# Kernel tuning notes

Measured on AMD Instinct MI355X. Metric: run time of the kernel, lower is better.

Reference implementation:

```python
import jax, jax.numpy as jnp
import numpy as np

M, K = 16384, 1024
E, N = 8, 5632  # N = 2 * intermediate (gate+up packed); intermediate = 2816
TOPK = 2


def setup_inputs() -> dict:
    key = jax.random.key(0)
    ks = jax.random.split(key, 5)
    return {
        "hidden_states": jax.random.normal(ks[0], (M, K), jnp.float32) * 0.05,
        "w1": jax.random.normal(ks[1], (E, N, K), jnp.float32) * 0.02,
        "w2": jax.random.normal(ks[2], (E, K, N // 2), jnp.float32) * 0.02,
        "topk_weights": jax.random.uniform(ks[3], (M, TOPK), jnp.float32),
        "topk_ids": jax.random.randint(ks[4], (M, TOPK), 0, E, jnp.int32),
    }


def reference(hidden_states, w1, w2, topk_weights, topk_ids):
    # hidden_states: [M, K]; w1: [E, N, K]; w2: [E, K, N//2]
    # topk_weights / topk_ids: [M, TOPK]
    m, k = hidden_states.shape
    e_num, n, _ = w1.shape
    topk = topk_ids.shape[1]
    half = n // 2
    out = jnp.zeros((m, topk, k), dtype=hidden_states.dtype)
    # Loop over the small fixed set of experts; each iteration is a dense GEMM
    # masked by the routing assignment (faithful to the grouped-GEMM math).
    for e in range(e_num):
        h1 = jnp.einsum('mk,nk->mn', hidden_states, w1[e])          # [M, N]
        gate, up = h1[:, :half], h1[:, half:]
        h2 = jax.nn.silu(gate) * up                                  # silu_and_mul
        o = jnp.einsum('mh,kh->mk', h2, w2[e])                       # [M, K]
        mask = (topk_ids == e).astype(o.dtype)                       # [M, TOPK]
        out = out + mask[:, :, None] * o[:, None, :]
    # multiply routed weights and sum over top-k slots
    return jnp.einsum('mtk,mt->mk', out, topk_weights)
```

## Files before the change

kernel.cpp:

```cpp
#include <hip/hip_runtime.h>
#include <hip/hip_bf16.h>

#define M_TOK 16384
#define K_DIM 1024
#define E_NUM 8
#define N_DIM 5632
#define HALF_N 2816
#define TOPK 2
#define NPAIR (M_TOK * TOPK)
#define BM 128
#define BK 64
#define BH1 128
#define BN 128
#define NDESC (NPAIR / BM + E_NUM)
#define NHB1 (HALF_N / BH1)
#define NNB2 (K_DIM / BN)

typedef short s16x4 __attribute__((ext_vector_type(4)));
typedef short s16x8 __attribute__((ext_vector_type(8)));
typedef float f32x4 __attribute__((ext_vector_type(4)));

__device__ __forceinline__ short f2bf(float f) {
  union { __hip_bfloat16 h; short s; } c;
  c.h = __float2bfloat16(f);
  return c.s;
}

__device__ __forceinline__ float bf2f(unsigned short s) {
  union { float f; unsigned u; } c;
  c.u = ((unsigned)s) << 16;
  return c.f;
}

__device__ __forceinline__ void gload_lds16(const void* g, void* l) {
  __builtin_amdgcn_global_load_lds(
      (const __attribute__((address_space(1))) unsigned int*)g,
      (__attribute__((address_space(3))) unsigned int*)l, 16, 0, 0);
}

__device__ __forceinline__ int xcd_work(int bid, int nwg) {
  const int xcd = bid & 7, loc = bid >> 3;
  const int q = nwg >> 3, r = nwg & 7;
  return (xcd < r ? xcd * (q + 1) : r * (q + 1) + (xcd - r) * q) + loc;
}

__global__ void cvt_f32_bf16_k(const float4* __restrict__ src,
                               s16x4* __restrict__ dst, int n4) {
  int i = blockIdx.x * blockDim.x + threadIdx.x;
  int stride = gridDim.x * blockDim.x;
  for (; i < n4; i += stride) {
    float4 f = src[i];
    s16x4 o = { f2bf(f.x), f2bf(f.y), f2bf(f.z), f2bf(f.w) };
    dst[i] = o;
  }
}

__global__ void moe_count(const int* __restrict__ ids, int* __restrict__ cnt) {
  const int p = blockIdx.x * 256 + threadIdx.x;
  const int e = ids[p];
  const int lane = threadIdx.x & 63;
  __shared__ int h[E_NUM];
  if (threadIdx.x < E_NUM) h[threadIdx.x] = 0;
  __syncthreads();
#pragma unroll
  for (int ex = 0; ex < E_NUM; ++ex) {
    unsigned long long m = __ballot(e == ex);
    if (lane == 0 && m) atomicAdd(&h[ex], __popcll(m));
  }
  __syncthreads();
  if (threadIdx.x < E_NUM) atomicAdd(&cnt[threadIdx.x], h[threadIdx.x]);
}

__global__ void moe_build(const int* __restrict__ cnt, int* __restrict__ offs,
                          int4* __restrict__ desc) {
  if (blockIdx.x == 0 && threadIdx.x == 0) {
    int o = 0, d = 0;
    for (int e = 0; e < E_NUM; ++e) {
      offs[e] = o;
      int end = o + cnt[e];
      for (int s = o; s < end; s += BM) desc[d++] = make_int4(e, s, end, 0);
      o = end;
    }
    offs[E_NUM] = o;
    while (d < NDESC) desc[d++] = make_int4(-1, 0, 0, 0);
  }
}

__global__ void moe_scatter(const int* __restrict__ ids, const float* __restrict__ tw,
                            const int* __restrict__ offs, int* __restrict__ fill,
                            int* __restrict__ tok, float* __restrict__ wgt,
                            int* __restrict__ inv) {
  const int p = blockIdx.x * 256 + threadIdx.x;
  const int e = ids[p];
  const int lane = threadIdx.x & 63;
  const int w = threadIdx.x >> 6;
  __shared__ int wcnt[4][E_NUM];
  __shared__ int wpre[4][E_NUM];
  __shared__ int base[E_NUM];
  const unsigned long long lt = (1ull << lane) - 1ull;
  int myrank = 0;
#pragma unroll
  for (int ex = 0; ex < E_NUM; ++ex) {
    unsigned long long m = __ballot(e == ex);
    if (e == ex) myrank = (int)__popcll(m & lt);
    if (lane == 0) wcnt[w][ex] = (int)__popcll(m);
  }
  __syncthreads();
  if (threadIdx.x < E_NUM) {
    const int ex = threadIdx.x;
    int s = 0;
#pragma unroll
    for (int ww = 0; ww < 4; ++ww) { wpre[ww][ex] = s; s += wcnt[ww][ex]; }
    base[ex] = atomicAdd(&fill[ex], s);
  }
  __syncthreads();
  const int pos = offs[e] + base[e] + wpre[w][e] + myrank;
  tok[pos] = p >> 1;
  wgt[pos] = tw[p];
  inv[p] = pos;
}

__global__ void moe_gather(const float* __restrict__ hs, const int* __restrict__ tok,
                           unsigned short* __restrict__ hsb) {
  const int pos = blockIdx.x;
  const int m = tok[pos];
  const int t = threadIdx.x;
  const float4* s = (const float4*)(hs + (size_t)m * K_DIM) + t * 2;
  const float4 a = s[0], b = s[1];
  s16x8 o = { f2bf(a.x), f2bf(a.y), f2bf(a.z), f2bf(a.w),
              f2bf(b.x), f2bf(b.y), f2bf(b.z), f2bf(b.w) };
  *(s16x8*)(hsb + (size_t)pos * K_DIM + t * 8) = o;
}

__launch_bounds__(512)
__global__ void moe_gemm1(const unsigned short* __restrict__ hsb,
                          const unsigned short* __restrict__ w1b,
                          const int4* __restrict__ desc,
                          unsigned short* __restrict__ h2) {
  const int work = xcd_work(blockIdx.x, NHB1 * NDESC);
  const int di = work / NHB1;
  const int hb = work - di * NHB1;
  const int4 d = desc[di];
  const int e = d.x;
  if (e < 0) return;
  const int pos0 = d.y, eend = d.z;
  const int h0 = hb * BH1;

  __shared__ __align__(16) unsigned short As[BM * BK];
  __shared__ __align__(16) unsigned short Gs[BH1 * BK];
  __shared__ __align__(16) unsigned short Us[BH1 * BK];

  const int tid = threadIdx.x;
  const int lane = tid & 63;
  const int wid = tid >> 6;
  const int wr = wid >> 1;
  const int wc = wid & 1;

  const unsigned short* Ab = hsb + (size_t)pos0 * K_DIM;
  const unsigned short* Gb = w1b + ((size_t)e * N_DIM + h0) * K_DIM;
  const unsigned short* Ub = Gb + (size_t)HALF_N * K_DIM;

  f32x4 accg[2][4], accu[2][4];
  const f32x4 z = {0.f, 0.f, 0.f, 0.f};
#pragma unroll
  for (int i = 0; i < 2; ++i)
#pragma unroll
    for (int j = 0; j < 4; ++j) { accg[i][j] = z; accu[i][j] = z; }

  const int lrow = lane >> 3;
  const int scol = ((lane & 7) ^ lrow) << 3;
  const int fr = lane & 15;
  const int fq = lane >> 4;
  const int sw = fr & 7;

  for (int kt = 0; kt < K_DIM / BK; ++kt) {
    const int k0 = kt * BK;
#pragma unroll
    for (int c = 0; c < 2; ++c) {
      const int seg = c * 8 + wid;
      const int row = seg * 8 + lrow;
      gload_lds16(Ab + (size_t)row * K_DIM + k0 + scol, &As[seg * 512]);
      gload_lds16(Gb + (size_t)row * K_DIM + k0 + scol, &Gs[seg * 512]);
      gload_lds16(Ub + (size_t)row * K_DIM + k0 + scol, &Us[seg * 512]);
    }
    __syncthreads();
#pragma unroll
    for (int s = 0; s < 2; ++s) {
      const int coff = (((s * 4 + fq) ^ sw) << 3);
      s16x8 af[2];
#pragma unroll
      for (int i = 0; i < 2; ++i)
        af[i] = *(const s16x8*)&As[(32 * wr + 16 * i + fr) * BK + coff];
#pragma unroll
      for (int j = 0; j < 4; ++j) {
        const int hr = (64 * wc + 16 * j + fr) * BK + coff;
        s16x8 gf = *(const s16x8*)&Gs[hr];
        s16x8 uf = *(const s16x8*)&Us[hr];
#pragma unroll
        for (int i = 0; i < 2; ++i) {
          accg[i][j] = __builtin_amdgcn_mfma_f32_16x16x32_bf16(af[i], gf, accg[i][j], 0, 0, 0);
          accu[i][j] = __builtin_amdgcn_mfma_f32_16x16x32_bf16(af[i], uf, accu[i][j], 0, 0, 0);
        }
      }
    }
    __syncthreads();
  }

  const int vlim = eend - pos0;
#pragma unroll
  for (int i = 0; i < 2; ++i) {
#pragma unroll
    for (int rr = 0; rr < 4; ++rr) {
      const int row = 32 * wr + 16 * i + fq * 4 + rr;
      if (row < vlim) {
        unsigned short* dst = h2 + (size_t)(pos0 + row) * HALF_N + h0 + 64 * wc;
#pragma unroll
        for (int j = 0; j < 4; ++j) {
          const float g = accg[i][j][rr];
          const float u = accu[i][j][rr];
          const float sg = g / (1.0f + __expf(-g));
          dst[16 * j + fr] = (unsigned short)f2bf(sg * u);
        }
      }
    }
  }
}

__launch_bounds__(256)
__global__ void moe_gemm2(const unsigned short* __restrict__ h2,
                          const unsigned short* __restrict__ w2b,
                          const int4* __restrict__ desc,
                          const float* __restrict__ wgt,
                          unsigned short* __restrict__ opair) {
  const int work = xcd_work(blockIdx.x, NNB2 * NDESC);
  const int di = work >> 3;
  const int nb = work & 7;
  const int4 d = desc[di];
  const int e = d.x;
  if (e < 0) return;
  const int pos0 = d.y, eend = d.z;
  const int n0 = nb * BN;

  __shared__ __align__(16) unsigned short As[BM * BK];
  __shared__ __align__(16) unsigned short Bs[BN * BK];

  const int tid = threadIdx.x;
  const int lane = tid & 63;
  const int wid = tid >> 6;
  const int wr = wid >> 1, wc = wid & 1;

  const unsigned short* Ab = h2 + (size_t)pos0 * HALF_N;
  const unsigned short* Bb = w2b + ((size_t)e * K_DIM + n0) * HALF_N;

  f32x4 acc[4][4];
  const f32x4 z = {0.f, 0.f, 0.f, 0.f};
#pragma unroll
  for (int i = 0; i < 4; ++i)
#pragma unroll
    for (int j = 0; j < 4; ++j) acc[i][j] = z;

  const int lrow = lane >> 3;
  const int scol = ((lane & 7) ^ lrow) << 3;
  const int fr = lane & 15;
  const int fq = lane >> 4;
  const int sw = fr & 7;

  for (int ht = 0; ht < HALF_N / BK; ++ht) {
    const int k0 = ht * BK;
#pragma unroll
    for (int c = 0; c < 4; ++c) {
      const int seg = c * 4 + wid;
      const int row = seg * 8 + lrow;
      gload_lds16(Ab + (size_t)row * HALF_N + k0 + scol, &As[seg * 512]);
      gload_lds16(Bb + (size_t)row * HALF_N + k0 + scol, &Bs[seg * 512]);
    }
    __syncthreads();
#pragma unroll
    for (int s = 0; s < 2; ++s) {
      const int coff = (((s * 4 + fq) ^ sw) << 3);
      s16x8 af[4], bf[4];
#pragma unroll
      for (int i = 0; i < 4; ++i)
        af[i] = *(const s16x8*)&As[(64 * wr + 16 * i + fr) * BK + coff];
#pragma unroll
      for (int j = 0; j < 4; ++j)
        bf[j] = *(const s16x8*)&Bs[(64 * wc + 16 * j + fr) * BK + coff];
#pragma unroll
      for (int i = 0; i < 4; ++i)
#pragma unroll
        for (int j = 0; j < 4; ++j)
          acc[i][j] = __builtin_amdgcn_mfma_f32_16x16x32_bf16(af[i], bf[j], acc[i][j], 0, 0, 0);
    }
    __syncthreads();
  }

  const int vlim = eend - pos0;
#pragma unroll
  for (int i = 0; i < 4; ++i) {
#pragma unroll
    for (int rr = 0; rr < 4; ++rr) {
      const int row = 64 * wr + 16 * i + fq * 4 + rr;
      if (row < vlim) {
        const int pos = pos0 + row;
        const float wt = wgt[pos];
        unsigned short* dst = opair + (size_t)pos * K_DIM + n0 + 64 * wc;
#pragma unroll
        for (int j = 0; j < 4; ++j)
          dst[16 * j + fr] = (unsigned short)f2bf(wt * acc[i][j][rr]);
      }
    }
  }
}

__global__ void moe_combine(const unsigned short* __restrict__ opair,
                            const int* __restrict__ inv,
                            float* __restrict__ out) {
  const int m = blockIdx.x;
  const int t = threadIdx.x;
  const int p0 = inv[2 * m], p1 = inv[2 * m + 1];
  const s16x8 a = *(const s16x8*)&opair[(size_t)p0 * K_DIM + t * 8];
  const s16x8 b = *(const s16x8*)&opair[(size_t)p1 * K_DIM + t * 8];
  float4 o0, o1;
  o0.x = bf2f((unsigned short)a[0]) + bf2f((unsigned short)b[0]);
  o0.y = bf2f((unsigned short)a[1]) + bf2f((unsigned short)b[1]);
  o0.z = bf2f((unsigned short)a[2]) + bf2f((unsigned short)b[2]);
  o0.w = bf2f((unsigned short)a[3]) + bf2f((unsigned short)b[3]);
  o1.x = bf2f((unsigned short)a[4]) + bf2f((unsigned short)b[4]);
  o1.y = bf2f((unsigned short)a[5]) + bf2f((unsigned short)b[5]);
  o1.z = bf2f((unsigned short)a[6]) + bf2f((unsigned short)b[6]);
  o1.w = bf2f((unsigned short)a[7]) + bf2f((unsigned short)b[7]);
  float4* dst = (float4*)(out + (size_t)m * K_DIM + t * 8);
  dst[0] = o0;
  dst[1] = o1;
}

__global__ void sentinel_k(float* o) { o[0] = 1.0e9f; }

extern "C" void kernel_launch(void* const* d_in, const int* in_sizes, int n_in,
                              void* d_out, int out_size, void* d_ws, size_t ws_size,
                              hipStream_t stream) {
  const float* hs = (const float*)d_in[0];
  const float* w1 = (const float*)d_in[1];
  const float* w2 = (const float*)d_in[2];
  const float* tw = (const float*)d_in[3];
  const int* ids = (const int*)d_in[4];
  float* out = (float*)d_out;

  char* p = (char*)d_ws;
  auto carve = [&](size_t bytes) {
    char* r = p;
    p += (bytes + 255) & ~(size_t)255;
    return r;
  };
  unsigned short* w1b = (unsigned short*)carve((size_t)E_NUM * N_DIM * K_DIM * 2);
  unsigned short* w2b = (unsigned short*)carve((size_t)E_NUM * K_DIM * HALF_N * 2);
  unsigned short* hsb = (unsigned short*)carve((size_t)(NPAIR + BM) * K_DIM * 2);
  unsigned short* h2  = (unsigned short*)carve((size_t)(NPAIR + BM) * HALF_N * 2);
  int*   tok  = (int*)carve(NPAIR * 4);
  float* wgt  = (float*)carve(NPAIR * 4);
  int*   inv  = (int*)carve(NPAIR * 4);
  int*   meta = (int*)carve(1024);
  int4*  desc = (int4*)carve(NDESC * sizeof(int4));
  size_t need = (size_t)(p - (char*)d_ws);

  unsigned short* opair = hsb;

  if (need > ws_size) {
    hipMemsetAsync(d_out, 0, (size_t)out_size * sizeof(float), stream);
    sentinel_k<<<1, 1, 0, stream>>>(out);
    return;
  }

  int* cnt  = meta;
  int* fill = meta + 64;
  int* offs = meta + 128;

  hipMemsetAsync(meta, 0, 1024, stream);

  cvt_f32_bf16_k<<<2048, 256, 0, stream>>>(
      (const float4*)w1, (s16x4*)w1b, (int)((size_t)E_NUM * N_DIM * K_DIM / 4));
  cvt_f32_bf16_k<<<2048, 256, 0, stream>>>(
      (const float4*)w2, (s16x4*)w2b, (int)((size_t)E_NUM * K_DIM * HALF_N / 4));
  moe_count<<<NPAIR / 256, 256, 0, stream>>>(ids, cnt);
  moe_build<<<1, 64, 0, stream>>>(cnt, offs, desc);
  moe_scatter<<<NPAIR / 256, 256, 0, stream>>>(ids, tw, offs, fill, tok, wgt, inv);
  moe_gather<<<NPAIR, 128, 0, stream>>>(hs, tok, hsb);
  moe_gemm1<<<NHB1 * NDESC, 512, 0, stream>>>(hsb, w1b, desc, h2);
  moe_gemm2<<<NNB2 * NDESC, 256, 0, stream>>>(h2, w2b, desc, wgt, opair);
  moe_combine<<<M_TOK, 128, 0, stream>>>(opair, inv, out);
}
```

Measured before the change: 915.7 us.

## Multi-buffer LDS in both MoE GEMMs to overlap global loads with MFMA

Gemm1 now uses triple-buffered LDS tiles and gemm2 double-buffered tiles. The next tiles are prefetched with direct global-to-LDS loads while MFMA runs on the current tile, and explicit s_waitcnt vmcnt counts plus raw barriers replace the load/sync/compute/sync loop. The goal is to hide global memory latency behind compute. In exchange LDS use grows (about 144KB for gemm1), which can cut occupancy, and correctness depends on the hand-set vmcnt values matching the number of loads issued.

```diff
diff --git a/kernel.cpp b/kernel.cpp
--- a/kernel.cpp
+++ b/kernel.cpp
@@ -146,9 +146,9 @@
   const int pos0 = d.y, eend = d.z;
   const int h0 = hb * BH1;
 
-  __shared__ __align__(16) unsigned short As[BM * BK];
-  __shared__ __align__(16) unsigned short Gs[BH1 * BK];
-  __shared__ __align__(16) unsigned short Us[BH1 * BK];
+  __shared__ __align__(16) unsigned short As[3][BM * BK];
+  __shared__ __align__(16) unsigned short Gs[3][BH1 * BK];
+  __shared__ __align__(16) unsigned short Us[3][BH1 * BK];
 
   const int tid = threadIdx.x;
   const int lane = tid & 63;
@@ -173,29 +173,49 @@
   const int fq = lane >> 4;
   const int sw = fr & 7;
 
-  for (int kt = 0; kt < K_DIM / BK; ++kt) {
+  auto STAGE = [&](int b, int kt) {
     const int k0 = kt * BK;
 #pragma unroll
     for (int c = 0; c < 2; ++c) {
       const int seg = c * 8 + wid;
       const int row = seg * 8 + lrow;
-      gload_lds16(Ab + (size_t)row * K_DIM + k0 + scol, &As[seg * 512]);
-      gload_lds16(Gb + (size_t)row * K_DIM + k0 + scol, &Gs[seg * 512]);
-      gload_lds16(Ub + (size_t)row * K_DIM + k0 + scol, &Us[seg * 512]);
-    }
-    __syncthreads();
+      gload_lds16(Ab + (size_t)row * K_DIM + k0 + scol, &As[b][seg * 512]);
+      gload_lds16(Gb + (size_t)row * K_DIM + k0 + scol, &Gs[b][seg * 512]);
+      gload_lds16(Ub + (size_t)row * K_DIM + k0 + scol, &Us[b][seg * 512]);
+    }
+  };
+
+  const int NKT = K_DIM / BK;
+  STAGE(0, 0);
+  STAGE(1, 1);
+  int b = 0;
+  for (int kt = 0; kt < NKT; ++kt) {
+    __builtin_amdgcn_s_barrier();
+    __builtin_amdgcn_sched_barrier(0);
+    if (kt + 2 < NKT) {
+      int nb = b + 2; if (nb >= 3) nb -= 3;
+      STAGE(nb, kt + 2);
+      asm volatile("s_waitcnt vmcnt(12)" ::: "memory");
+    } else if (kt + 1 < NKT) {
+      asm volatile("s_waitcnt vmcnt(6)" ::: "memory");
+    } else {
+      asm volatile("s_waitcnt vmcnt(0)" ::: "memory");
+    }
+    __builtin_amdgcn_s_barrier();
+    __builtin_amdgcn_sched_barrier(0);
+
 #pragma unroll
     for (int s = 0; s < 2; ++s) {
       const int coff = (((s * 4 + fq) ^ sw) << 3);
       s16x8 af[2];
 #pragma unroll
       for (int i = 0; i < 2; ++i)
-        af[i] = *(const s16x8*)&As[(32 * wr + 16 * i + fr) * BK + coff];
+        af[i] = *(const s16x8*)&As[b][(32 * wr + 16 * i + fr) * BK + coff];
 #pragma unroll
       for (int j = 0; j < 4; ++j) {
         const int hr = (64 * wc + 16 * j + fr) * BK + coff;
-        s16x8 gf = *(const s16x8*)&Gs[hr];
-        s16x8 uf = *(const s16x8*)&Us[hr];
+        s16x8 gf = *(const s16x8*)&Gs[b][hr];
+        s16x8 uf = *(const s16x8*)&Us[b][hr];
 #pragma unroll
         for (int i = 0; i < 2; ++i) {
           accg[i][j] = __builtin_amdgcn_mfma_f32_16x16x32_bf16(af[i], gf, accg[i][j], 0, 0, 0);
@@ -203,7 +223,7 @@
         }
       }
     }
-    __syncthreads();
+    ++b; if (b >= 3) b -= 3;
   }
 
   const int vlim = eend - pos0;
@@ -241,8 +261,8 @@
   const int pos0 = d.y, eend = d.z;
   const int n0 = nb * BN;
 
-  __shared__ __align__(16) unsigned short As[BM * BK];
-  __shared__ __align__(16) unsigned short Bs[BN * BK];
+  __shared__ __align__(16) unsigned short As[2][BM * BK];
+  __shared__ __align__(16) unsigned short Bs[2][BN * BK];
 
   const int tid = threadIdx.x;
   const int lane = tid & 63;
@@ -265,33 +285,48 @@
   const int fq = lane >> 4;
   const int sw = fr & 7;
 
-  for (int ht = 0; ht < HALF_N / BK; ++ht) {
+  auto STAGE = [&](int b, int ht) {
     const int k0 = ht * BK;
 #pragma unroll
     for (int c = 0; c < 4; ++c) {
       const int seg = c * 4 + wid;
       const int row = seg * 8 + lrow;
-      gload_lds16(Ab + (size_t)row * HALF_N + k0 + scol, &As[seg * 512]);
-      gload_lds16(Bb + (size_t)row * HALF_N + k0 + scol, &Bs[seg * 512]);
-    }
-    __syncthreads();
+      gload_lds16(Ab + (size_t)row * HALF_N + k0 + scol, &As[b][seg * 512]);
+      gload_lds16(Bb + (size_t)row * HALF_N + k0 + scol, &Bs[b][seg * 512]);
+    }
+  };
+
+  const int NKT = HALF_N / BK;
+  STAGE(0, 0);
+  for (int ht = 0; ht < NKT; ++ht) {
+    const int b = ht & 1;
+    __builtin_amdgcn_s_barrier();
+    __builtin_amdgcn_sched_barrier(0);
+    if (ht + 1 < NKT) {
+      STAGE(b ^ 1, ht + 1);
+      asm volatile("s_waitcnt vmcnt(8)" ::: "memory");
+    } else {
+      asm volatile("s_waitcnt vmcnt(0)" ::: "memory");
+    }
+    __builtin_amdgcn_s_barrier();
+    __builtin_amdgcn_sched_barrier(0);
+
 #pragma unroll
     for (int s = 0; s < 2; ++s) {
       const int coff = (((s * 4 + fq) ^ sw) << 3);
       s16x8 af[4], bf[4];
 #pragma unroll
       for (int i = 0; i < 4; ++i)
-        af[i] = *(const s16x8*)&As[(64 * wr + 16 * i + fr) * BK + coff];
+        af[i] = *(const s16x8*)&As[b][(64 * wr + 16 * i + fr) * BK + coff];
 #pragma unroll
       for (int j = 0; j < 4; ++j)
-        bf[j] = *(const s16x8*)&Bs[(64 * wc + 16 * j + fr) * BK + coff];
+        bf[j] = *(const s16x8*)&Bs[b][(64 * wc + 16 * j + fr) * BK + coff];
 #pragma unroll
       for (int i = 0; i < 4; ++i)
 #pragma unroll
         for (int j = 0; j < 4; ++j)
           acc[i][j] = __builtin_amdgcn_mfma_f32_16x16x32_bf16(af[i], bf[j], acc[i][j], 0, 0, 0);
     }
-    __syncthreads();
   }
 
   const int vlim = eend - pos0;
```

Measured after the change: 1.029 ms. 12.4% more time.
